# Kernel tuning notes

Hardware: AMD Instinct MI355X
Metric: run time of the kernel (lower is better)

## Reference

```python
import jax, jax.numpy as jnp
import numpy as np

EMBED_DIM = 768
NUM_HEADS = 12
HEAD_DIM = EMBED_DIM // NUM_HEADS


def setup_inputs() -> dict:
    key = jax.random.key(0)
    k_x, k_qkv_w, k_qkv_b, k_pw, k_pb = jax.random.split(key, 5)
    B, S = 16, 1024
    scale = 1.0 / np.sqrt(EMBED_DIM)
    return {
        "x": jax.random.normal(k_x, (B, S, EMBED_DIM), dtype=jnp.float32),
        "qkv_w": jax.random.normal(k_qkv_w, (EMBED_DIM, 3 * EMBED_DIM), dtype=jnp.float32) * scale,
        "qkv_b": jax.random.normal(k_qkv_b, (3 * EMBED_DIM,), dtype=jnp.float32) * 0.02,
        "proj_w": jax.random.normal(k_pw, (EMBED_DIM, EMBED_DIM), dtype=jnp.float32) * scale,
        "proj_b": jax.random.normal(k_pb, (EMBED_DIM,), dtype=jnp.float32) * 0.02,
    }


def reference(x, qkv_w, qkv_b, proj_w, proj_b):
    B, S, E = x.shape
    H, D = NUM_HEADS, HEAD_DIM
    qkv = x @ qkv_w + qkv_b                      # [B, S, 3E]
    qkv = qkv.reshape(B, S, 3, H, D)
    qkv = jnp.transpose(qkv, (2, 0, 3, 1, 4))    # [3, B, H, S, D]
    q, k, v = qkv[0], qkv[1], qkv[2]
    scores = jnp.einsum("bhqd,bhkd->bhqk", q, k) / jnp.sqrt(jnp.float32(D))
    probs = jax.nn.softmax(scores, axis=-1)      # dropout is identity in eval
    attn = jnp.einsum("bhqk,bhkd->bhqd", probs, v)
    attn = jnp.transpose(attn, (0, 2, 1, 3)).reshape(B, S, E)
    return attn @ proj_w + proj_b
```

## Files before the change

kernel.cpp:

```cpp
#include <hip/hip_runtime.h>
#include <hip/hip_bf16.h>

typedef unsigned short u16;
typedef short s16x8 __attribute__((ext_vector_type(8)));
typedef float f32x4 __attribute__((ext_vector_type(4)));

#define EMB 768
#define NH 12
#define HD 64
#define BB 16
#define SS 1024
#define MTOK (BB*SS)
#define NQKV (3*EMB)
#define QSZ ((size_t)BB*NH*SS*HD)

#define GLOBAL_AS const __attribute__((address_space(1))) void*
#define LDS_AS __attribute__((address_space(3))) void*

#if __has_builtin(__builtin_amdgcn_exp2f)
#define EXP2(x) __builtin_amdgcn_exp2f(x)
#else
#define EXP2(x) exp2f(x)
#endif

__device__ __forceinline__ u16 f2bf(float f){
  unsigned u = __float_as_uint(f);
  u += 0x7FFFu + ((u >> 16) & 1u);
  return (u16)(u >> 16);
}
__device__ __forceinline__ u16 f2bf_trunc(float f){
  return (u16)(__float_as_uint(f) >> 16);
}
__device__ __forceinline__ f32x4 mfma16(s16x8 a, s16x8 b, f32x4 c){
  return __builtin_amdgcn_mfma_f32_16x16x32_bf16(a, b, c, 0, 0, 0);
}

#define NBA 12288
#define NBB 1728
#define NBC 576

__device__ __forceinline__ void transpose_body(
    u16 (*tile)[33], const float* __restrict__ in, u16* __restrict__ out,
    int R, int C, int bxi, int byi){
  int bx = bxi * 32, by = byi * 32;
  int tx = threadIdx.x & 31, ty = threadIdx.x >> 5;
  #pragma unroll
  for(int i = 0; i < 32; i += 8)
    tile[ty + i][tx] = f2bf(in[(size_t)(by + ty + i) * C + bx + tx]);
  __syncthreads();
  #pragma unroll
  for(int i = 0; i < 32; i += 8)
    out[(size_t)(bx + ty + i) * R + by + tx] = tile[tx][ty + i];
}

__global__ __launch_bounds__(256) void prep_kernel(
    const float4* __restrict__ x4, ushort4* __restrict__ xb4,
    const float* __restrict__ qkv_w, u16* __restrict__ qkv_wT,
    const float* __restrict__ proj_w, u16* __restrict__ proj_wT){
  __shared__ u16 tile[32][33];
  int bid = blockIdx.x;
  if(bid < NBA){
    int i = bid * 256 + threadIdx.x;
    float4 f = x4[i];
    ushort4 o;
    o.x = f2bf(f.x); o.y = f2bf(f.y); o.z = f2bf(f.z); o.w = f2bf(f.w);
    xb4[i] = o;
  } else if(bid < NBA + NBB){
    int bi = bid - NBA;
    transpose_body(tile, qkv_w, qkv_wT, EMB, NQKV, bi % (NQKV/32), bi / (NQKV/32));
  } else {
    int bi = bid - NBA - NBB;
    transpose_body(tile, proj_w, proj_wT, EMB, EMB, bi % (EMB/32), bi / (EMB/32));
  }
}

template<int MODE>
__device__ __forceinline__ void gemm_body(
    const u16* __restrict__ A, const u16* __restrict__ Bt,
    const float* __restrict__ bias,
    void* __restrict__ out0, u16* __restrict__ out1, u16* __restrict__ out2){
  const int K = 768, NT = 12;
  __shared__ u16 As[2][256*64];
  __shared__ u16 Bs[2][256*64];
  int tid = threadIdx.x;

  int gx = gridDim.x;
  int nwg = gx * gridDim.y;
  int L = blockIdx.y * gx + blockIdx.x;
  int nl = (L & 7) * (nwg >> 3) + (L >> 3);
  int m0 = (nl / gx) * 256, n0 = (nl % gx) * 256;

  int w = tid >> 6, lane = tid & 63, quad = lane >> 4, l15 = lane & 15;
  int wm = (w >> 2) * 128, wn = (w & 3) * 64;
  int rr = lane >> 3;
  int cp = lane & 7;
  f32x4 acc[8][4] = {};

  auto stageQ = [&](int t, int q){
    int d = t & 1, k0 = t * 64;
    const u16* src = (q < 2) ? A : Bt;
    int base = (q < 2) ? m0 : n0;
    u16* dst = (q < 2) ? As[d] : Bs[d];
    int h = q & 1;
    #pragma unroll
    for(int it = 0; it < 2; ++it){
      int ci = h*16 + it*8 + w;
      int r  = ci * 8 + rr;
      int gc = (cp ^ (r & 7)) * 8;
      __builtin_amdgcn_global_load_lds(
          (GLOBAL_AS)(src + (size_t)(base + r) * K + k0 + gc),
          (LDS_AS)(dst + ci * 512 + lane * 8), 16, 0, 0);
    }
  };

  s16x8 a[8], b0[4], b1[4];
  auto dsA = [&](int d, int mh){
    #pragma unroll
    for(int kk = 0; kk < 2; ++kk){
      int ch = ((kk*4 + quad) ^ (l15 & 7)) * 8;
      #pragma unroll
      for(int i = 0; i < 4; ++i)
        a[kk*4+i] = *(const s16x8*)&As[d][(wm + (mh*4+i)*16 + l15) * 64 + ch];
    }
  };
  auto dsB = [&](int d, int nh, s16x8* bb){
    #pragma unroll
    for(int kk = 0; kk < 2; ++kk){
      int ch = ((kk*4 + quad) ^ (l15 & 7)) * 8;
      #pragma unroll
      for(int j = 0; j < 2; ++j)
        bb[kk*2+j] = *(const s16x8*)&Bs[d][(wn + (nh*2+j)*16 + l15) * 64 + ch];
    }
  };
  auto mfmaQ = [&](int mh, int nh, const s16x8* bb){
    __builtin_amdgcn_s_setprio(1);
    #pragma unroll
    for(int kk = 0; kk < 2; ++kk)
      #pragma unroll
      for(int i = 0; i < 4; ++i)
        #pragma unroll
        for(int j = 0; j < 2; ++j)
          acc[mh*4+i][nh*2+j] = mfma16(a[kk*4+i], bb[kk*2+j], acc[mh*4+i][nh*2+j]);
    __builtin_amdgcn_s_setprio(0);
  };

#define PHASE_SYNC() do{ \
    __builtin_amdgcn_s_barrier(); \
    asm volatile("s_waitcnt lgkmcnt(0)" ::: "memory"); \
    __builtin_amdgcn_sched_barrier(0); \
  }while(0)
#define PHASE_END() do{ \
    __builtin_amdgcn_s_barrier(); \
    __builtin_amdgcn_sched_barrier(0); \
  }while(0)

  stageQ(0,0); stageQ(0,1); stageQ(0,2); stageQ(0,3);
  stageQ(1,0);
  asm volatile("s_waitcnt vmcnt(2)" ::: "memory");
  __builtin_amdgcn_s_barrier();
  __builtin_amdgcn_sched_barrier(0);

  #pragma unroll
  for(int j = 0; j < NT/2; ++j){
    int t = 2*j;
    stageQ(t+1, 1);
    dsA(0, 0); dsB(0, 0, b0);
    PHASE_SYNC(); mfmaQ(0, 0, b0); PHASE_END();
    stageQ(t+1, 2);
    dsB(0, 1, b1);
    PHASE_SYNC(); mfmaQ(0, 1, b1); PHASE_END();
    stageQ(t+1, 3);
    dsA(0, 1);
    PHASE_SYNC(); mfmaQ(1, 0, b0); PHASE_END();
    if(t+2 < NT){ stageQ(t+2, 0); asm volatile("s_waitcnt vmcnt(2)" ::: "memory"); }
    else        { asm volatile("s_waitcnt vmcnt(0)" ::: "memory"); }
    PHASE_SYNC(); mfmaQ(1, 1, b1); PHASE_END();
    if(t+2 < NT) stageQ(t+2, 1);
    dsA(1, 0); dsB(1, 0, b0);
    PHASE_SYNC(); mfmaQ(0, 0, b0); PHASE_END();
    if(t+2 < NT) stageQ(t+2, 2);
    dsB(1, 1, b1);
    PHASE_SYNC(); mfmaQ(0, 1, b1); PHASE_END();
    if(t+2 < NT) stageQ(t+2, 3);
    dsA(1, 1);
    PHASE_SYNC(); mfmaQ(1, 0, b0); PHASE_END();
    if(t+3 < NT){ stageQ(t+3, 0); asm volatile("s_waitcnt vmcnt(2)" ::: "memory"); }
    else if(t+2 < NT){ asm volatile("s_waitcnt vmcnt(0)" ::: "memory"); }
    PHASE_SYNC(); mfmaQ(1, 1, b1); PHASE_END();
  }
#undef PHASE_SYNC
#undef PHASE_END

  #pragma unroll
  for(int mt = 0; mt < 8; ++mt){
    #pragma unroll
    for(int nt = 0; nt < 4; ++nt){
      int n = n0 + wn + nt*16 + l15;
      float bv = bias[n];
      #pragma unroll
      for(int r = 0; r < 4; ++r){
        int m = m0 + wm + mt*16 + quad*4 + r;
        float v = acc[mt][nt][r] + bv;
        if(MODE == 1){
          ((float*)out0)[(size_t)m * EMB + n] = v;
        } else {
          u16 hv = f2bf(v);
          int which = n / EMB, rem = n - which * EMB;
          int h = rem >> 6, d = rem & 63;
          int bb = m >> 10, ss = m & 1023;
          size_t bh = (size_t)(bb * NH + h);
          if(which == 0)      ((u16*)out0)[(bh * SS + ss) * HD + d] = hv;
          else if(which == 1) out1[(bh * SS + ss) * HD + d] = hv;
          else                out2[(bh * HD + d) * SS + ss] = hv;
        }
      }
    }
  }
}

__global__ __launch_bounds__(512, 2) void qkv_gemm_kernel(
    const u16* __restrict__ A, const u16* __restrict__ Bt,
    const float* __restrict__ bias,
    u16* __restrict__ Qo, u16* __restrict__ Ko, u16* __restrict__ Vo){
  gemm_body<0>(A, Bt, bias, Qo, Ko, Vo);
}
__global__ __launch_bounds__(512, 2) void proj_gemm_kernel(
    const u16* __restrict__ A, const u16* __restrict__ Bt,
    const float* __restrict__ bias, float* __restrict__ out){
  gemm_body<1>(A, Bt, bias, out, nullptr, nullptr);
}

__global__ __launch_bounds__(256) void attn_kernel(
    const u16* __restrict__ Qws, const u16* __restrict__ Kws,
    const u16* __restrict__ Vtws, u16* __restrict__ attn){
  __shared__ u16 Ks[2][64*64];
  __shared__ u16 Vs[2][64*64];
  __shared__ __align__(16) u16 Ps[4][2][16][76];
  int tid = threadIdx.x;
  int w = tid >> 6, lane = tid & 63, quad = lane >> 4, l15 = lane & 15;
  int bh = blockIdx.x;
  int b = bh / NH, h = bh - b * NH;
  int q0 = blockIdx.y * 128 + w * 32;
  const u16* Qbase = Qws  + (size_t)bh * SS * HD;
  const u16* Kbase = Kws  + (size_t)bh * SS * HD;
  const u16* Vbase = Vtws + (size_t)bh * HD * SS;

  s16x8 aq[2][2];
  #pragma unroll
  for(int m = 0; m < 2; m++){
    int qrow = q0 + m*16 + l15;
    #pragma unroll
    for(int kk = 0; kk < 2; kk++)
      aq[m][kk] = *(const s16x8*)(Qbase + (size_t)qrow * HD + kk*32 + quad*8);
  }

  f32x4 o[2][4] = {};
  float psum[2][4] = {};
  const float C1 = 0.125f * 1.44269504f;
  const float C0 = -30.0f * 1.44269504f;

  int krr = lane >> 3, kcp = lane & 7;

  auto stageKV = [&](int p, int kt){
    #pragma unroll
    for(int it = 0; it < 2; ++it){
      int ins = it * 4 + w;
      int r   = ins * 8 + krr;
      int gck = (kcp ^ (r & 7)) * 8;
      __builtin_amdgcn_global_load_lds(
          (GLOBAL_AS)(Kbase + (size_t)(kt*64 + r) * HD + gck),
          (LDS_AS)(Ks[p] + ins * 512 + lane * 8), 16, 0, 0);
      __builtin_amdgcn_global_load_lds(
          (GLOBAL_AS)(Vbase + (size_t)r * SS + kt*64 + gck),
          (LDS_AS)(Vs[p] + ins * 512 + lane * 8), 16, 0, 0);
    }
  };

  stageKV(0, 0);
  int p = 0;
  for(int kt = 0; kt < 16; ++kt){
    __syncthreads();
    if(kt < 15) stageKV(p ^ 1, kt + 1);

    #pragma unroll
    for(int nt = 0; nt < 4; ++nt){
      s16x8 bk[2];
      #pragma unroll
      for(int kk = 0; kk < 2; kk++){
        int ch = ((kk*4 + quad) ^ (l15 & 7)) * 8;
        bk[kk] = *(const s16x8*)&Ks[p][(nt*16 + l15) * 64 + ch];
      }
      #pragma unroll
      for(int m = 0; m < 2; m++){
        f32x4 z = {};
        z = mfma16(aq[m][0], bk[0], z);
        z = mfma16(aq[m][1], bk[1], z);
        #pragma unroll
        for(int r = 0; r < 4; r++){
          float pv = EXP2(z[r] * C1 + C0);
          psum[m][r] += pv;
          Ps[w][m][quad*4 + r][nt*16 + l15] = f2bf_trunc(pv);
        }
      }
    }
    #pragma unroll
    for(int k4 = 0; k4 < 2; k4++){
      s16x8 pa[2];
      #pragma unroll
      for(int m = 0; m < 2; m++)
        pa[m] = *(const s16x8*)&Ps[w][m][l15][k4*32 + quad*8];
      #pragma unroll
      for(int nt = 0; nt < 4; nt++){
        int ch = ((k4*4 + quad) ^ (l15 & 7)) * 8;
        s16x8 vb = *(const s16x8*)&Vs[p][(nt*16 + l15) * 64 + ch];
        #pragma unroll
        for(int m = 0; m < 2; m++)
          o[m][nt] = mfma16(pa[m], vb, o[m][nt]);
      }
    }
    p ^= 1;
  }

  #pragma unroll
  for(int m = 0; m < 2; m++){
    #pragma unroll
    for(int r = 0; r < 4; r++){
      float s = psum[m][r];
      s += __shfl_xor(s, 1, 64);
      s += __shfl_xor(s, 2, 64);
      s += __shfl_xor(s, 4, 64);
      s += __shfl_xor(s, 8, 64);
      float inv = 1.0f / s;
      int srow = q0 + m*16 + quad*4 + r;
      size_t base = ((size_t)(b * SS + srow)) * EMB + h * HD;
      #pragma unroll
      for(int nt = 0; nt < 4; nt++)
        attn[base + nt*16 + l15] = f2bf(o[m][nt][r] * inv);
    }
  }
}

extern "C" void kernel_launch(void* const* d_in, const int* in_sizes, int n_in,
                              void* d_out, int out_size, void* d_ws, size_t ws_size,
                              hipStream_t stream){
  const float* x      = (const float*)d_in[0];
  const float* qkv_w  = (const float*)d_in[1];
  const float* qkv_b  = (const float*)d_in[2];
  const float* proj_w = (const float*)d_in[3];
  const float* proj_b = (const float*)d_in[4];

  char* ws = (char*)d_ws;
  u16* qkv_wT  = (u16*)ws; ws += (size_t)NQKV * EMB * 2;
  u16* proj_wT = (u16*)ws; ws += (size_t)EMB * EMB * 2;
  u16* x_bf = (u16*)ws; ws += QSZ * 2;
  u16* Qws  = (u16*)ws; ws += QSZ * 2;
  u16* Kws  = (u16*)ws; ws += QSZ * 2;
  u16* Vtws = (u16*)ws; ws += QSZ * 2;
  u16* attn = x_bf;

  prep_kernel<<<NBA + NBB + NBC, 256, 0, stream>>>(
      (const float4*)x, (ushort4*)x_bf, qkv_w, qkv_wT, proj_w, proj_wT);
  qkv_gemm_kernel<<<dim3(NQKV/256, MTOK/256), 512, 0, stream>>>(
      x_bf, qkv_wT, qkv_b, Qws, Kws, Vtws);
  attn_kernel<<<dim3(BB*NH, SS/128), 256, 0, stream>>>(Qws, Kws, Vtws, attn);
  proj_gemm_kernel<<<dim3(EMB/256, MTOK/256), 512, 0, stream>>>(
      attn, proj_wT, proj_b, (float*)d_out);
}
```

Measured before the change: 316.3 us.

## Split QKV GEMM into simpler 128x128 kernel and transpose score MFMA in attention

```diff
diff --git a/kernel.cpp b/kernel.cpp
--- a/kernel.cpp
+++ b/kernel.cpp
@@ -2,6 +2,7 @@
 #include <hip/hip_bf16.h>
 
 typedef unsigned short u16;
+typedef unsigned int u32;
 typedef short s16x8 __attribute__((ext_vector_type(8)));
 typedef float f32x4 __attribute__((ext_vector_type(4)));
 
@@ -74,11 +75,91 @@
   }
 }
 
-template<int MODE>
-__device__ __forceinline__ void gemm_body(
+__global__ __launch_bounds__(256) void qkv_gemm_kernel(
     const u16* __restrict__ A, const u16* __restrict__ Bt,
     const float* __restrict__ bias,
-    void* __restrict__ out0, u16* __restrict__ out1, u16* __restrict__ out2){
+    u16* __restrict__ Qo, u16* __restrict__ Ko, u16* __restrict__ Vo){
+  const int K = 768;
+  __shared__ u16 As[2][128*64];
+  __shared__ u16 Bs[2][128*64];
+  int tid = threadIdx.x;
+
+  int gx = gridDim.x;
+  int nwg = gx * gridDim.y;
+  int L = blockIdx.y * gx + blockIdx.x;
+  int nl = (L & 7) * (nwg >> 3) + (L >> 3);
+  int m0 = (nl / gx) * 128, n0 = (nl % gx) * 128;
+
+  int w = tid >> 6, lane = tid & 63, quad = lane >> 4, l15 = lane & 15;
+  int wm = (w >> 1) * 64, wn = (w & 1) * 64;
+  int rr = lane >> 3;
+  int cp = lane & 7;
+  f32x4 acc[4][4] = {};
+
+  auto stage = [&](int p, int k0){
+    #pragma unroll
+    for(int it = 0; it < 4; ++it){
+      int ci = it * 4 + w;
+      int r  = ci * 8 + rr;
+      int gc = (cp ^ (r & 7)) * 8;
+      __builtin_amdgcn_global_load_lds(
+          (GLOBAL_AS)(A + (size_t)(m0 + r) * K + k0 + gc),
+          (LDS_AS)(As[p] + ci * 512 + lane * 8), 16, 0, 0);
+      __builtin_amdgcn_global_load_lds(
+          (GLOBAL_AS)(Bt + (size_t)(n0 + r) * K + k0 + gc),
+          (LDS_AS)(Bs[p] + ci * 512 + lane * 8), 16, 0, 0);
+    }
+  };
+
+  stage(0, 0);
+  int p = 0;
+  for(int k0 = 0; k0 < K; k0 += 64){
+    __syncthreads();
+    if(k0 + 64 < K) stage(p ^ 1, k0 + 64);
+    #pragma unroll
+    for(int kk = 0; kk < 2; kk++){
+      s16x8 a[4], b[4];
+      int ch = ((kk * 4 + quad) ^ (l15 & 7)) * 8;
+      #pragma unroll
+      for(int i = 0; i < 4; i++){
+        a[i] = *(const s16x8*)&As[p][(wm + i*16 + l15) * 64 + ch];
+        b[i] = *(const s16x8*)&Bs[p][(wn + i*16 + l15) * 64 + ch];
+      }
+      #pragma unroll
+      for(int mt = 0; mt < 4; mt++)
+        #pragma unroll
+        for(int nt = 0; nt < 4; nt++)
+          acc[mt][nt] = mfma16(a[mt], b[nt], acc[mt][nt]);
+    }
+    p ^= 1;
+  }
+
+  #pragma unroll
+  for(int mt = 0; mt < 4; mt++){
+    #pragma unroll
+    for(int nt = 0; nt < 4; nt++){
+      int n = n0 + wn + nt*16 + l15;
+      float bv = bias[n];
+      #pragma unroll
+      for(int r = 0; r < 4; r++){
+        int m = m0 + wm + mt*16 + quad*4 + r;
+        float v = acc[mt][nt][r] + bv;
+        u16 hv = f2bf(v);
+        int which = n / EMB, rem = n - which * EMB;
+        int h = rem >> 6, d = rem & 63;
+        int bb = m >> 10, ss = m & 1023;
+        size_t bh = (size_t)(bb * NH + h);
+        if(which == 0)      Qo[(bh * SS + ss) * HD + d] = hv;
+        else if(which == 1) Ko[(bh * SS + ss) * HD + d] = hv;
+        else                Vo[(bh * HD + d) * SS + ss] = hv;
+      }
+    }
+  }
+}
+
+__global__ __launch_bounds__(512, 2) void proj_gemm_kernel(
+    const u16* __restrict__ A, const u16* __restrict__ Bt,
+    const float* __restrict__ bias, float* __restrict__ out){
   const int K = 768, NT = 12;
   __shared__ u16 As[2][256*64];
   __shared__ u16 Bs[2][256*64];
@@ -200,34 +281,10 @@
       #pragma unroll
       for(int r = 0; r < 4; ++r){
         int m = m0 + wm + mt*16 + quad*4 + r;
-        float v = acc[mt][nt][r] + bv;
-        if(MODE == 1){
-          ((float*)out0)[(size_t)m * EMB + n] = v;
-        } else {
-          u16 hv = f2bf(v);
-          int which = n / EMB, rem = n - which * EMB;
-          int h = rem >> 6, d = rem & 63;
-          int bb = m >> 10, ss = m & 1023;
-          size_t bh = (size_t)(bb * NH + h);
-          if(which == 0)      ((u16*)out0)[(bh * SS + ss) * HD + d] = hv;
-          else if(which == 1) out1[(bh * SS + ss) * HD + d] = hv;
-          else                out2[(bh * HD + d) * SS + ss] = hv;
-        }
-      }
-    }
-  }
-}
-
-__global__ __launch_bounds__(512, 2) void qkv_gemm_kernel(
-    const u16* __restrict__ A, const u16* __restrict__ Bt,
-    const float* __restrict__ bias,
-    u16* __restrict__ Qo, u16* __restrict__ Ko, u16* __restrict__ Vo){
-  gemm_body<0>(A, Bt, bias, Qo, Ko, Vo);
-}
-__global__ __launch_bounds__(512, 2) void proj_gemm_kernel(
-    const u16* __restrict__ A, const u16* __restrict__ Bt,
-    const float* __restrict__ bias, float* __restrict__ out){
-  gemm_body<1>(A, Bt, bias, out, nullptr, nullptr);
+        out[(size_t)m * EMB + n] = acc[mt][nt][r] + bv;
+      }
+    }
+  }
 }
 
 __global__ __launch_bounds__(256) void attn_kernel(
@@ -255,7 +312,7 @@
   }
 
   f32x4 o[2][4] = {};
-  float psum[2][4] = {};
+  float psum[2] = {};
   const float C1 = 0.125f * 1.44269504f;
   const float C0 = -30.0f * 1.44269504f;
 
@@ -293,14 +350,17 @@
       #pragma unroll
       for(int m = 0; m < 2; m++){
         f32x4 z = {};
-        z = mfma16(aq[m][0], bk[0], z);
-        z = mfma16(aq[m][1], bk[1], z);
-        #pragma unroll
-        for(int r = 0; r < 4; r++){
-          float pv = EXP2(z[r] * C1 + C0);
-          psum[m][r] += pv;
-          Ps[w][m][quad*4 + r][nt*16 + l15] = f2bf_trunc(pv);
-        }
+        z = mfma16(bk[0], aq[m][0], z);
+        z = mfma16(bk[1], aq[m][1], z);
+        float p0 = EXP2(z[0] * C1 + C0);
+        float p1 = EXP2(z[1] * C1 + C0);
+        float p2 = EXP2(z[2] * C1 + C0);
+        float p3 = EXP2(z[3] * C1 + C0);
+        psum[m] += (p0 + p1) + (p2 + p3);
+        uint2 pk;
+        pk.x = (u32)f2bf_trunc(p0) | ((u32)f2bf_trunc(p1) << 16);
+        pk.y = (u32)f2bf_trunc(p2) | ((u32)f2bf_trunc(p3) << 16);
+        *(uint2*)&Ps[w][m][l15][nt*16 + quad*4] = pk;
       }
     }
     #pragma unroll
@@ -323,14 +383,12 @@
 
   #pragma unroll
   for(int m = 0; m < 2; m++){
+    float s = psum[m];
+    s += __shfl_xor(s, 16, 64);
+    s += __shfl_xor(s, 32, 64);
     #pragma unroll
     for(int r = 0; r < 4; r++){
-      float s = psum[m][r];
-      s += __shfl_xor(s, 1, 64);
-      s += __shfl_xor(s, 2, 64);
-      s += __shfl_xor(s, 4, 64);
-      s += __shfl_xor(s, 8, 64);
-      float inv = 1.0f / s;
+      float inv = 1.0f / __shfl(s, quad*4 + r, 64);
       int srow = q0 + m*16 + quad*4 + r;
       size_t base = ((size_t)(b * SS + srow)) * EMB + h * HD;
       #pragma unroll
@@ -360,7 +418,7 @@
 
   prep_kernel<<<NBA + NBB + NBC, 256, 0, stream>>>(
       (const float4*)x, (ushort4*)x_bf, qkv_w, qkv_wT, proj_w, proj_wT);
-  qkv_gemm_kernel<<<dim3(NQKV/256, MTOK/256), 512, 0, stream>>>(
+  qkv_gemm_kernel<<<dim3(NQKV/128, MTOK/128), 256, 0, stream>>>(
       x_bf, qkv_wT, qkv_b, Qws, Kws, Vtws);
   attn_kernel<<<dim3(BB*NH, SS/128), 256, 0, stream>>>(Qws, Kws, Vtws, attn);
   proj_gemm_kernel<<<dim3(EMB/256, MTOK/256), 512, 0, stream>>>(
```

Measured after the change: 314.7 us. No clear change (-0.5%).
